# Optimization experiments

Hardware: AMD Instinct MI355X
Metric: run time of the kernel (lower is better)

The kernel has to match this reference:

```python
import jax, jax.numpy as jnp
import numpy as np

T, B, I, H, NH, O = 2048, 256, 64, 128, 512, 64


def setup_inputs() -> dict:
    key = jax.random.key(0)
    ks = jax.random.split(key, 9)
    s = 1.0 / np.sqrt(H)
    return {
        "x": jax.random.normal(ks[0], (T, B, I), dtype=jnp.float32),
        "W_ih": jax.random.uniform(ks[1], (4 * H, I), jnp.float32, -s, s),
        "W_hh": jax.random.uniform(ks[2], (4 * H, H), jnp.float32, -s, s),
        "b_ih": jax.random.uniform(ks[3], (4 * H,), jnp.float32, -s, s),
        "b_hh": jax.random.uniform(ks[4], (4 * H,), jnp.float32, -s, s),
        "W1": jax.random.uniform(ks[5], (NH, H), jnp.float32, -1 / np.sqrt(H), 1 / np.sqrt(H)),
        "b1": jax.random.uniform(ks[6], (NH,), jnp.float32, -1 / np.sqrt(H), 1 / np.sqrt(H)),
        "W2": jax.random.uniform(ks[7], (O, NH), jnp.float32, -1 / np.sqrt(NH), 1 / np.sqrt(NH)),
        "b2": jax.random.uniform(ks[8], (O,), jnp.float32, -1 / np.sqrt(NH), 1 / np.sqrt(NH)),
    }


def lstm_scan(x, W_ih, W_hh, b_ih, b_hh):
    Bsz = x.shape[1]
    Hd = W_hh.shape[1]
    # precompute input projection for all timesteps: [T, B, 4H]
    xg = jnp.einsum('tbi,gi->tbg', x, W_ih) + (b_ih + b_hh)

    def step(carry, xg_t):
        h, c = carry
        gates = xg_t + h @ W_hh.T  # [B, 4H]
        i, f, g, o = jnp.split(gates, 4, axis=-1)  # PyTorch gate order
        i = jax.nn.sigmoid(i)
        f = jax.nn.sigmoid(f)
        g = jnp.tanh(g)
        o = jax.nn.sigmoid(o)
        c = f * c + i * g
        h = o * jnp.tanh(c)
        return (h, c), h

    h0 = jnp.zeros((Bsz, Hd), x.dtype)
    c0 = jnp.zeros((Bsz, Hd), x.dtype)
    (hT, cT), hs = jax.lax.scan(step, (h0, c0), xg)
    return hs, hT, cT


def reference(x, W_ih, W_hh, b_ih, b_hh, W1, b1, W2, b2):
    hs, hT, cT = lstm_scan(x, W_ih, W_hh, b_ih, b_hh)  # hs: [T, B, H]
    out = jax.nn.relu(jnp.einsum('tbh,nh->tbn', hs, W1) + b1)
    out = jnp.einsum('tbn,on->tbo', out, W2) + b2
    # hidden returned as (h_n, c_n) with n_layers leading dim = 1
    return out, (hT[None], cT[None])
```

## Files before the change

### kernel.cpp

```cpp
#include <hip/hip_runtime.h>
#include <hip/hip_bf16.h>

#define TT 2048
#define BB 256
#define II 64
#define HH 128
#define GG 512
#define NHH 512
#define OO 64

#define OSTRIDE 520
#define W2STRIDE 520
#define XSTRIDE 72
#define GSTRIDE 516

typedef _Float16 h2    __attribute__((ext_vector_type(2)));
typedef _Float16 half4 __attribute__((ext_vector_type(4)));
typedef _Float16 half8 __attribute__((ext_vector_type(8)));
typedef float f32x4    __attribute__((ext_vector_type(4)));

__device__ __forceinline__ float sigm(float x) {
    return __builtin_amdgcn_rcpf(1.f + __expf(-x));
}
__device__ __forceinline__ float tanh_f(float x) {
    float e = __expf(-2.f * fabsf(x));
    float t = (1.f - e) * __builtin_amdgcn_rcpf(1.f + e);
    return copysignf(t, x);
}
__device__ __forceinline__ void sync_lds() {
    __builtin_amdgcn_s_waitcnt(0xC07F);
    __builtin_amdgcn_s_barrier();
}

__global__ void prep_kernel(const float* __restrict__ W1, const float* __restrict__ W2,
                            _Float16* __restrict__ W1h, _Float16* __restrict__ W2h)
{
    int tid = blockIdx.x * blockDim.x + threadIdx.x;
    int n = gridDim.x * blockDim.x;
    for (int i = tid; i < NHH * HH; i += n) W1h[i] = (_Float16)W1[i];
    for (int i = tid; i < OO * NHH; i += n) W2h[i] = (_Float16)W2[i];
}

__global__ __launch_bounds__(512, 2) void lstm_scan9(
    const float* __restrict__ x,
    const float* __restrict__ W_ih, const float* __restrict__ W_hh,
    const float* __restrict__ b_ih, const float* __restrict__ b_hh,
    _Float16* __restrict__ hs, float* __restrict__ out_tail)
{
    __shared__ __align__(16) _Float16 hbuf[2][HH];
    __shared__ __align__(16) _Float16 xstage[2][16 * XSTRIDE];
    __shared__ __align__(16) _Float16 xgw[2][16 * GSTRIDE];

    const int tid  = threadIdx.x;
    const int wv   = tid >> 6;
    const int lane = tid & 63;
    const int lrow = lane & 15;
    const int q    = lane >> 4;
    const int b    = blockIdx.x;
    const int col  = wv * 16 + lrow;

    if (tid < 2 * HH) ((_Float16*)hbuf)[tid] = (_Float16)0.f;

    half8 Bh[4][4], Bx[4][2];
    float biasv[4];
    int colg[4];
    #pragma unroll
    for (int g = 0; g < 4; ++g) {
        int n = g * HH + col;
        colg[g] = n;
        biasv[g] = b_ih[n] + b_hh[n];
        #pragma unroll
        for (int kt = 0; kt < 4; ++kt) {
            const float* p = W_hh + (size_t)n * HH + kt * 32 + q * 8;
            float4 f0 = *(const float4*)p;
            float4 f1 = *(const float4*)(p + 4);
            half8 bb = {(_Float16)f0.x, (_Float16)f0.y, (_Float16)f0.z, (_Float16)f0.w,
                        (_Float16)f1.x, (_Float16)f1.y, (_Float16)f1.z, (_Float16)f1.w};
            Bh[g][kt] = bb;
        }
        #pragma unroll
        for (int kt = 0; kt < 2; ++kt) {
            const float* p = W_ih + (size_t)n * II + kt * 32 + q * 8;
            float4 f0 = *(const float4*)p;
            float4 f1 = *(const float4*)(p + 4);
            half8 bb = {(_Float16)f0.x, (_Float16)f0.y, (_Float16)f0.z, (_Float16)f0.w,
                        (_Float16)f1.x, (_Float16)f1.y, (_Float16)f1.z, (_Float16)f1.w};
            Bx[g][kt] = bb;
        }
    }

    #pragma unroll
    for (int j = 0; j < 2; ++j) {
        int e = tid + j * 512, r = e >> 6, c2 = e & 63;
        xstage[0][r * XSTRIDE + c2] = (_Float16)x[((size_t)r * BB + b) * II + c2];
    }
    __syncthreads();
    {
        half8 Ax0 = *(const half8*)&xstage[0][lrow * XSTRIDE + q * 8];
        half8 Ax1 = *(const half8*)&xstage[0][lrow * XSTRIDE + 32 + q * 8];
        #pragma unroll
        for (int g = 0; g < 4; ++g) {
            f32x4 Cg = {biasv[g], biasv[g], biasv[g], biasv[g]};
            Cg = __builtin_amdgcn_mfma_f32_16x16x32_f16(Ax0, Bx[g][0], Cg, 0, 0, 0);
            Cg = __builtin_amdgcn_mfma_f32_16x16x32_f16(Ax1, Bx[g][1], Cg, 0, 0, 0);
            #pragma unroll
            for (int reg = 0; reg < 4; ++reg)
                xgw[0][(q * 4 + reg) * GSTRIDE + colg[g]] = (_Float16)Cg[reg];
        }
    }
    float xr0, xr1;
    {
        int r0 = tid >> 6, c0 = tid & 63;
        int r1 = (tid + 512) >> 6, c1 = tid & 63;
        xr0 = x[((size_t)(16 + r0) * BB + b) * II + c0];
        xr1 = x[((size_t)(16 + r1) * BB + b) * II + c1];
    }
    __syncthreads();

    float cst = 0.f, hlast = 0.f;
    _Float16* hp = hs + (size_t)b * HH + col;

    for (int t = 0; t < TT; ++t) {
        const int par   = t & 1;
        const int wp    = (t >> 4) & 1;
        const int phase = t & 15;
        const _Float16* hb = hbuf[par];

        half8 Af[4];
        #pragma unroll
        for (int kt = 0; kt < 4; ++kt)
            Af[kt] = *(const half8*)&hb[kt * 32 + q * 8];

        float seed[4];
        #pragma unroll
        for (int g = 0; g < 4; ++g)
            seed[g] = (float)xgw[wp][phase * GSTRIDE + colg[g]];

        if (phase == 0 && t + 16 < TT) {
            int r0 = tid >> 6, c0 = tid & 63;
            int r1 = (tid + 512) >> 6, c1 = tid & 63;
            xstage[wp ^ 1][r0 * XSTRIDE + c0] = (_Float16)xr0;
            xstage[wp ^ 1][r1 * XSTRIDE + c1] = (_Float16)xr1;
            if (t + 32 < TT) {
                xr0 = x[((size_t)(t + 32 + r0) * BB + b) * II + c0];
                xr1 = x[((size_t)(t + 32 + r1) * BB + b) * II + c1];
            }
        }
        if (phase == 8 && t + 8 < TT) {
            const _Float16* xs = xstage[wp ^ 1];
            half8 Ax0 = *(const half8*)&xs[lrow * XSTRIDE + q * 8];
            half8 Ax1 = *(const half8*)&xs[lrow * XSTRIDE + 32 + q * 8];
            #pragma unroll
            for (int g = 0; g < 4; ++g) {
                f32x4 Cg = {biasv[g], biasv[g], biasv[g], biasv[g]};
                Cg = __builtin_amdgcn_mfma_f32_16x16x32_f16(Ax0, Bx[g][0], Cg, 0, 0, 0);
                Cg = __builtin_amdgcn_mfma_f32_16x16x32_f16(Ax1, Bx[g][1], Cg, 0, 0, 0);
                #pragma unroll
                for (int reg = 0; reg < 4; ++reg)
                    xgw[wp ^ 1][(q * 4 + reg) * GSTRIDE + colg[g]] = (_Float16)Cg[reg];
            }
        }

        f32x4 Ca[4], Cb[4];
        #pragma unroll
        for (int g = 0; g < 4; ++g) {
            f32x4 ci = {seed[g], 0.f, 0.f, 0.f};
            Ca[g] = ci;
            f32x4 z = {0.f, 0.f, 0.f, 0.f};
            Cb[g] = z;
        }
        #pragma unroll
        for (int kt = 0; kt < 2; ++kt)
            #pragma unroll
            for (int g = 0; g < 4; ++g)
                Ca[g] = __builtin_amdgcn_mfma_f32_16x16x32_f16(Af[kt], Bh[g][kt], Ca[g], 0, 0, 0);
        #pragma unroll
        for (int kt = 2; kt < 4; ++kt)
            #pragma unroll
            for (int g = 0; g < 4; ++g)
                Cb[g] = __builtin_amdgcn_mfma_f32_16x16x32_f16(Af[kt], Bh[g][kt], Cb[g], 0, 0, 0);

        if (lane < 16) {
            float gi = Ca[0][0] + Cb[0][0];
            float gf = Ca[1][0] + Cb[1][0];
            float gg = Ca[2][0] + Cb[2][0];
            float go = Ca[3][0] + Cb[3][0];
            cst = sigm(gf) * cst + sigm(gi) * tanh_f(gg);
            float hn = sigm(go) * tanh_f(cst);
            hlast = hn;
            _Float16 hf = (_Float16)hn;
            hbuf[par ^ 1][col] = hf;
            *hp = hf;
        }
        hp += (size_t)BB * HH;
        sync_lds();
    }

    if (lane < 16) {
        out_tail[(size_t)b * HH + col] = hlast;
        out_tail[(size_t)BB * HH + (size_t)b * HH + col] = cst;
    }
}

__global__ __launch_bounds__(512, 2) void head_mfma4(
    const _Float16* __restrict__ hs,
    const _Float16* __restrict__ W1h, const float* __restrict__ b1,
    const _Float16* __restrict__ W2h, const float* __restrict__ b2,
    float* __restrict__ out)
{
    __shared__ __align__(16) _Float16 o1[64 * OSTRIDE];
    __shared__ __align__(16) _Float16 w2s[64 * W2STRIDE];

    const int tid = threadIdx.x, wv = tid >> 6, lane = tid & 63;
    const int lrow = lane & 15, q = lane >> 4;

    for (int i = tid; i < OO * NHH; i += 512)
        w2s[(i >> 9) * W2STRIDE + (i & 511)] = W2h[i];

    half8 B1[4][4];
    float bias1[4];
    #pragma unroll
    for (int nt = 0; nt < 4; ++nt) {
        bias1[nt] = b1[wv * 64 + nt * 16 + lrow];
        #pragma unroll
        for (int kt = 0; kt < 4; ++kt)
            B1[nt][kt] = *(const half8*)&W1h[(wv * 64 + nt * 16 + lrow) * HH + kt * 32 + q * 8];
    }
    const int mt2 = wv >> 1;
    const int nh0 = (wv & 1) * 2;
    float bias2[2] = {b2[nh0 * 16 + lrow], b2[(nh0 + 1) * 16 + lrow]};

    const size_t row_base = (size_t)blockIdx.x * (32 * 64);

    half8 An[4];
    #pragma unroll
    for (int kt = 0; kt < 4; ++kt)
        An[kt] = *(const half8*)(hs + (row_base + lrow) * HH + kt * 32 + q * 8);

    __syncthreads();

    for (int tile = 0; tile < 32; ++tile) {
        const size_t rows0 = row_base + (size_t)tile * 64;

        #pragma unroll
        for (int mt = 0; mt < 4; ++mt) {
            half8 Ac[4];
            #pragma unroll
            for (int kt = 0; kt < 4; ++kt) Ac[kt] = An[kt];
            if (!(tile == 31 && mt == 3)) {
                size_t nrow = rows0 + (size_t)(mt + 1) * 16;
                #pragma unroll
                for (int kt = 0; kt < 4; ++kt)
                    An[kt] = *(const half8*)(hs + (nrow + lrow) * HH + kt * 32 + q * 8);
            }
            f32x4 C1[4];
            #pragma unroll
            for (int nt = 0; nt < 4; ++nt) {
                f32x4 ci = {bias1[nt], bias1[nt], bias1[nt], bias1[nt]};
                C1[nt] = ci;
            }
            #pragma unroll
            for (int kt = 0; kt < 4; ++kt)
                #pragma unroll
                for (int nt = 0; nt < 4; ++nt)
                    C1[nt] = __builtin_amdgcn_mfma_f32_16x16x32_f16(Ac[kt], B1[nt][kt], C1[nt], 0, 0, 0);
            #pragma unroll
            for (int nt = 0; nt < 4; ++nt)
                #pragma unroll
                for (int reg = 0; reg < 4; ++reg) {
                    float v = C1[nt][reg];
                    v = v > 0.f ? v : 0.f;
                    o1[(mt * 16 + q * 4 + reg) * OSTRIDE + wv * 64 + nt * 16 + lrow] = (_Float16)v;
                }
        }
        sync_lds();

        f32x4 C2a[2], C2b[2];
        #pragma unroll
        for (int j = 0; j < 2; ++j) {
            f32x4 ci = {bias2[j], bias2[j], bias2[j], bias2[j]};
            C2a[j] = ci;
            f32x4 z = {0.f, 0.f, 0.f, 0.f};
            C2b[j] = z;
        }
        #pragma unroll
        for (int kt = 0; kt < 16; ++kt) {
            half8 ua = *(const half8*)&o1[(mt2 * 16 + lrow) * OSTRIDE + kt * 32 + q * 8];
            #pragma unroll
            for (int j = 0; j < 2; ++j) {
                half8 ub = *(const half8*)&w2s[((nh0 + j) * 16 + lrow) * W2STRIDE + kt * 32 + q * 8];
                if (kt & 1) C2b[j] = __builtin_amdgcn_mfma_f32_16x16x32_f16(ua, ub, C2b[j], 0, 0, 0);
                else        C2a[j] = __builtin_amdgcn_mfma_f32_16x16x32_f16(ua, ub, C2a[j], 0, 0, 0);
            }
        }
        #pragma unroll
        for (int j = 0; j < 2; ++j)
            #pragma unroll
            for (int reg = 0; reg < 4; ++reg)
                out[(rows0 + mt2 * 16 + q * 4 + reg) * OO + (nh0 + j) * 16 + lrow] = C2a[j][reg] + C2b[j][reg];
        sync_lds();
    }
}

extern "C" void kernel_launch(void* const* d_in, const int* in_sizes, int n_in,
                              void* d_out, int out_size, void* d_ws, size_t ws_size,
                              hipStream_t stream)
{
    const float* x    = (const float*)d_in[0];
    const float* W_ih = (const float*)d_in[1];
    const float* W_hh = (const float*)d_in[2];
    const float* b_ih = (const float*)d_in[3];
    const float* b_hh = (const float*)d_in[4];
    const float* W1   = (const float*)d_in[5];
    const float* b1   = (const float*)d_in[6];
    const float* W2   = (const float*)d_in[7];
    const float* b2   = (const float*)d_in[8];
    float* out = (float*)d_out;

    char* ws = (char*)d_ws;
    _Float16* W1h = (_Float16*)(ws + 0);
    _Float16* W2h = (_Float16*)(ws + 131072);
    _Float16* hs  = (_Float16*)(ws + 196608);

    prep_kernel<<<64, 256, 0, stream>>>(W1, W2, W1h, W2h);

    float* tail = out + (size_t)TT * BB * OO;
    lstm_scan9<<<BB, 512, 0, stream>>>(x, W_ih, W_hh, b_ih, b_hh, hs, tail);

    head_mfma4<<<BB, 512, 0, stream>>>(hs, W1h, b1, W2h, b2, out);
}
```

Measured before the change: 1.551 ms.

## Unroll LSTM scan into 16-step windows and prefetch next gate seed

```diff
diff --git a/kernel.cpp b/kernel.cpp
--- a/kernel.cpp
+++ b/kernel.cpp
@@ -41,7 +41,7 @@
     for (int i = tid; i < OO * NHH; i += n) W2h[i] = (_Float16)W2[i];
 }
 
-__global__ __launch_bounds__(512, 2) void lstm_scan9(
+__global__ __launch_bounds__(512, 2) void lstm_scan10(
     const float* __restrict__ x,
     const float* __restrict__ W_ih, const float* __restrict__ W_hh,
     const float* __restrict__ b_ih, const float* __restrict__ b_hh,
@@ -109,95 +109,102 @@
         }
     }
     float xr0, xr1;
-    {
-        int r0 = tid >> 6, c0 = tid & 63;
-        int r1 = (tid + 512) >> 6, c1 = tid & 63;
-        xr0 = x[((size_t)(16 + r0) * BB + b) * II + c0];
-        xr1 = x[((size_t)(16 + r1) * BB + b) * II + c1];
-    }
+    const int xr_r0 = tid >> 6, xr_c = tid & 63;
+    const int xr_r1 = (tid + 512) >> 6;
+    xr0 = x[((size_t)(16 + xr_r0) * BB + b) * II + xr_c];
+    xr1 = x[((size_t)(16 + xr_r1) * BB + b) * II + xr_c];
     __syncthreads();
 
-    float cst = 0.f, hlast = 0.f;
+    _Float16 sc[4];
+    #pragma unroll
+    for (int g = 0; g < 4; ++g) sc[g] = xgw[0][colg[g]];
+
+    float cst = 0.f;
     _Float16* hp = hs + (size_t)b * HH + col;
 
-    for (int t = 0; t < TT; ++t) {
-        const int par   = t & 1;
-        const int wp    = (t >> 4) & 1;
-        const int phase = t & 15;
-        const _Float16* hb = hbuf[par];
-
-        half8 Af[4];
-        #pragma unroll
-        for (int kt = 0; kt < 4; ++kt)
-            Af[kt] = *(const half8*)&hb[kt * 32 + q * 8];
-
-        float seed[4];
-        #pragma unroll
-        for (int g = 0; g < 4; ++g)
-            seed[g] = (float)xgw[wp][phase * GSTRIDE + colg[g]];
-
-        if (phase == 0 && t + 16 < TT) {
-            int r0 = tid >> 6, c0 = tid & 63;
-            int r1 = (tid + 512) >> 6, c1 = tid & 63;
-            xstage[wp ^ 1][r0 * XSTRIDE + c0] = (_Float16)xr0;
-            xstage[wp ^ 1][r1 * XSTRIDE + c1] = (_Float16)xr1;
-            if (t + 32 < TT) {
-                xr0 = x[((size_t)(t + 32 + r0) * BB + b) * II + c0];
-                xr1 = x[((size_t)(t + 32 + r1) * BB + b) * II + c1];
-            }
-        }
-        if (phase == 8 && t + 8 < TT) {
-            const _Float16* xs = xstage[wp ^ 1];
-            half8 Ax0 = *(const half8*)&xs[lrow * XSTRIDE + q * 8];
-            half8 Ax1 = *(const half8*)&xs[lrow * XSTRIDE + 32 + q * 8];
+    for (int w = 0; w < TT / 16; ++w) {
+        const int wp = w & 1;
+        const _Float16* xgw_cur = xgw[wp];
+        const _Float16* xgw_nxt = xgw[wp ^ 1];
+
+        #pragma unroll
+        for (int phase = 0; phase < 16; ++phase) {
+            const int par = phase & 1;
+            const _Float16* hb = hbuf[par];
+
+            half8 Af[4];
+            #pragma unroll
+            for (int kt = 0; kt < 4; ++kt)
+                Af[kt] = *(const half8*)&hb[kt * 32 + q * 8];
+
+            _Float16 sn[4];
+            {
+                const _Float16* sp = (phase == 15) ? xgw_nxt : (xgw_cur + (phase + 1) * GSTRIDE);
+                #pragma unroll
+                for (int g = 0; g < 4; ++g) sn[g] = sp[colg[g]];
+            }
+
+            if (phase == 0) {
+                int t = w * 16;
+                if (t + 16 < TT) {
+                    xstage[wp ^ 1][xr_r0 * XSTRIDE + xr_c] = (_Float16)xr0;
+                    xstage[wp ^ 1][xr_r1 * XSTRIDE + xr_c] = (_Float16)xr1;
+                    if (t + 32 < TT) {
+                        xr0 = x[((size_t)(t + 32 + xr_r0) * BB + b) * II + xr_c];
+                        xr1 = x[((size_t)(t + 32 + xr_r1) * BB + b) * II + xr_c];
+                    }
+                }
+            }
+            if (phase == 8) {
+                if (w * 16 + 16 < TT) {
+                    const _Float16* xs = xstage[wp ^ 1];
+                    half8 Ax0 = *(const half8*)&xs[lrow * XSTRIDE + q * 8];
+                    half8 Ax1 = *(const half8*)&xs[lrow * XSTRIDE + 32 + q * 8];
+                    #pragma unroll
+                    for (int g = 0; g < 4; ++g) {
+                        f32x4 Cg = {biasv[g], biasv[g], biasv[g], biasv[g]};
+                        Cg = __builtin_amdgcn_mfma_f32_16x16x32_f16(Ax0, Bx[g][0], Cg, 0, 0, 0);
+                        Cg = __builtin_amdgcn_mfma_f32_16x16x32_f16(Ax1, Bx[g][1], Cg, 0, 0, 0);
+                        #pragma unroll
+                        for (int reg = 0; reg < 4; ++reg)
+                            xgw[wp ^ 1][(q * 4 + reg) * GSTRIDE + colg[g]] = (_Float16)Cg[reg];
+                    }
+                }
+            }
+
+            f32x4 C[4];
             #pragma unroll
             for (int g = 0; g < 4; ++g) {
-                f32x4 Cg = {biasv[g], biasv[g], biasv[g], biasv[g]};
-                Cg = __builtin_amdgcn_mfma_f32_16x16x32_f16(Ax0, Bx[g][0], Cg, 0, 0, 0);
-                Cg = __builtin_amdgcn_mfma_f32_16x16x32_f16(Ax1, Bx[g][1], Cg, 0, 0, 0);
-                #pragma unroll
-                for (int reg = 0; reg < 4; ++reg)
-                    xgw[wp ^ 1][(q * 4 + reg) * GSTRIDE + colg[g]] = (_Float16)Cg[reg];
-            }
-        }
-
-        f32x4 Ca[4], Cb[4];
-        #pragma unroll
-        for (int g = 0; g < 4; ++g) {
-            f32x4 ci = {seed[g], 0.f, 0.f, 0.f};
-            Ca[g] = ci;
-            f32x4 z = {0.f, 0.f, 0.f, 0.f};
-            Cb[g] = z;
-        }
-        #pragma unroll
-        for (int kt = 0; kt < 2; ++kt)
-            #pragma unroll
-            for (int g = 0; g < 4; ++g)
-                Ca[g] = __builtin_amdgcn_mfma_f32_16x16x32_f16(Af[kt], Bh[g][kt], Ca[g], 0, 0, 0);
-        #pragma unroll
-        for (int kt = 2; kt < 4; ++kt)
-            #pragma unroll
-            for (int g = 0; g < 4; ++g)
-                Cb[g] = __builtin_amdgcn_mfma_f32_16x16x32_f16(Af[kt], Bh[g][kt], Cb[g], 0, 0, 0);
-
-        if (lane < 16) {
-            float gi = Ca[0][0] + Cb[0][0];
-            float gf = Ca[1][0] + Cb[1][0];
-            float gg = Ca[2][0] + Cb[2][0];
-            float go = Ca[3][0] + Cb[3][0];
-            cst = sigm(gf) * cst + sigm(gi) * tanh_f(gg);
-            float hn = sigm(go) * tanh_f(cst);
-            hlast = hn;
-            _Float16 hf = (_Float16)hn;
-            hbuf[par ^ 1][col] = hf;
-            *hp = hf;
-        }
-        hp += (size_t)BB * HH;
-        sync_lds();
+                float s = (float)sc[g];
+                f32x4 ci = {s, s, s, s};
+                C[g] = ci;
+            }
+            #pragma unroll
+            for (int kt = 0; kt < 4; ++kt)
+                #pragma unroll
+                for (int g = 0; g < 4; ++g)
+                    C[g] = __builtin_amdgcn_mfma_f32_16x16x32_f16(Af[kt], Bh[g][kt], C[g], 0, 0, 0);
+
+            if (lane < 16) {
+                float gi = C[0][0];
+                float gf = C[1][0];
+                float gg = C[2][0];
+                float go = C[3][0];
+                cst = sigm(gf) * cst + sigm(gi) * tanh_f(gg);
+                float hn = sigm(go) * tanh_f(cst);
+                _Float16 hf = (_Float16)hn;
+                hbuf[par ^ 1][col] = hf;
+                *hp = hf;
+            }
+            hp += (size_t)BB * HH;
+            #pragma unroll
+            for (int g = 0; g < 4; ++g) sc[g] = sn[g];
+            sync_lds();
+        }
     }
 
     if (lane < 16) {
-        out_tail[(size_t)b * HH + col] = hlast;
+        out_tail[(size_t)b * HH + col] = (float)hbuf[0][col];
         out_tail[(size_t)BB * HH + (size_t)b * HH + col] = cst;
     }
 }
@@ -325,7 +332,7 @@
     prep_kernel<<<64, 256, 0, stream>>>(W1, W2, W1h, W2h);
 
     float* tail = out + (size_t)TT * BB * OO;
-    lstm_scan9<<<BB, 512, 0, stream>>>(x, W_ih, W_hh, b_ih, b_hh, hs, tail);
+    lstm_scan10<<<BB, 512, 0, stream>>>(x, W_ih, W_hh, b_ih, b_hh, hs, tail);
 
     head_mfma4<<<BB, 512, 0, stream>>>(hs, W1h, b1, W2h, b2, out);
 }
```

Result: faster. 1.362 ms (-12.2%).
